# Optimization experiments

Hardware: AMD Instinct MI355X
Metric: run time of the kernel (lower is better)

The kernel has to match this reference:

```python
import jax, jax.numpy as jnp
import numpy as np

TIME_WEIGHT = 0.1
CURRENT_TIME = 0.0

def setup_inputs() -> dict:
    key = jax.random.key(0)
    k1, k2, k3, k4, k5 = jax.random.split(key, 5)
    B, M, D, C = 131072, 100, 1024, 16
    return {
        "query": jax.random.normal(k1, (B, D), dtype=jnp.float32),
        "context": jax.random.normal(k2, (B, C), dtype=jnp.float32),
        "mem_keys": jax.random.normal(k3, (M, D), dtype=jnp.float32),
        "mem_values": jax.random.normal(k4, (M, D), dtype=jnp.float32),
        "mem_contexts": jax.random.normal(k5, (M, C), dtype=jnp.float32),
        "mem_timestamps": jnp.zeros((M, 1), dtype=jnp.float32),
    }

def reference(query, context, mem_keys, mem_values, mem_contexts, mem_timestamps):
    # content scores: [B, M]
    scores = jnp.einsum('bd,md->bm', query, mem_keys)
    # contextual binding
    scores = scores + 0.5 * jnp.einsum('bc,mc->bm', context, mem_contexts)
    # exponential time-decay bias, broadcast over batch: [M]
    time_decay = jnp.exp(-TIME_WEIGHT * (CURRENT_TIME - mem_timestamps.squeeze(-1)))
    scores = scores + time_decay[None, :]
    attn = jax.nn.softmax(scores, axis=-1)
    return jnp.einsum('bm,md->bd', attn, mem_values)
```

## Files before the change

kernel.cpp:

```cpp
#include <hip/hip_runtime.h>


typedef __attribute__((ext_vector_type(8))) _Float16 f16x8;
typedef __attribute__((ext_vector_type(4))) float f32x4;

constexpr int DQ = 1024, CD = 16, MM = 100, KD = 1056, NT = 7;
constexpr size_t KE = (size_t)112 * KD;

constexpr int KOFF = 8192, KBUF = 7168;
constexpr int VOFF = 32768, VBUF = 8192;
constexpr int LDSZ = 57344;

#define WAITV(n) asm volatile("s_waitcnt vmcnt(" #n ")" ::: "memory")

__device__ __forceinline__ void gl16(const void* g, void* l) {
    __builtin_amdgcn_global_load_lds(
        (const __attribute__((address_space(1))) unsigned int*)g,
        (__attribute__((address_space(3))) unsigned int*)l, 16, 0, 0);
}

__global__ void build_k(const float* __restrict__ mk, const float* __restrict__ mc,
                        _Float16* __restrict__ KH)
{
    int d = blockIdx.x * 64 + threadIdx.x;
    int m = blockIdx.y;
    if (d >= KD) return;
    float x = 0.f;
    if (m < MM) {
        if (d < DQ)            x = mk[(size_t)m * DQ + d];
        else if (d < DQ + CD)  x = 0.5f * mc[(size_t)m * CD + (d - DQ)];
    }
    KH[(size_t)m * KD + d] = (_Float16)x;
}

__global__ void build_vt(const float* __restrict__ mv, _Float16* __restrict__ VT)
{
    int idx = blockIdx.x * 256 + threadIdx.x;
    int d = idx >> 7, m = idx & 127;
    VT[idx] = (m < MM) ? (_Float16)mv[(size_t)m * DQ + d] : (_Float16)0.f;
}

__global__ __launch_bounds__(512, 4)
void epmem_pipe(const float* __restrict__ q, const float* __restrict__ cx,
                const float* __restrict__ ts,
                const _Float16* __restrict__ KH, const _Float16* __restrict__ VT,
                float* __restrict__ out)
{
    __shared__ __align__(16) char lds[LDSZ];

    const int t = threadIdx.x, w = t >> 6, lane = t & 63;
    const int lr = lane & 15, lk = lane >> 4;
    const int row0 = blockIdx.x * 128;

    float dec[NT];
    #pragma unroll
    for (int nt = 0; nt < NT; ++nt) {
        int m = nt * 16 + lr;
        dec[nt] = (m < MM) ? __expf(0.1f * ts[m]) : 0.f;
    }

    auto stageCtx = [&]() {
        gl16(cx + (size_t)(row0 + (t >> 2)) * CD + (t & 3) * 4, lds + (w * 64) * 16);
    };
    auto stageK = [&](int buf, int ks) {
        if (w < 7) {
            char* dst = lds + KOFF + buf * KBUF;
            int s = w * 64 + lane;
            int m = s >> 2;
            int logical = (s & 3) ^ ((m >> 1) & 3);
            gl16(KH + (size_t)m * KD + ks * 32 + logical * 8, dst + (w * 64) * 16);
        }
    };
    auto stageV = [&](int buf, int c) {
        char* dst = lds + VOFF + buf * VBUF;
        int d = t >> 4;
        int logical = (t & 15) ^ (d & 15);
        gl16(VT + (size_t)(c * 32 + d) * 128 + logical * 8, dst + (w * 64) * 16);
    };

    f32x4 acc[NT];
    #pragma unroll
    for (int nt = 0; nt < NT; ++nt) acc[nt] = (f32x4){0.f, 0.f, 0.f, 0.f};

    const float* qp = q + (size_t)(row0 + w * 16 + lr) * DQ + 8 * lk;

    auto qkStep = [&](f32x4 x, f32x4 y, int ks) {
        f16x8 ah, al;
        #pragma unroll
        for (int e = 0; e < 4; ++e) {
            _Float16 h = (_Float16)x[e]; ah[e] = h;     al[e] = (_Float16)(x[e] - (float)h);
            h = (_Float16)y[e];          ah[4 + e] = h; al[4 + e] = (_Float16)(y[e] - (float)h);
        }
        const char* kb = lds + KOFF + (ks % 3) * KBUF;
        #pragma unroll
        for (int nt = 0; nt < NT; ++nt) {
            int m = nt * 16 + lr;
            f16x8 bh = *(const f16x8*)(kb + ((m << 2) + (lk ^ ((lr >> 1) & 3))) * 16);
            acc[nt] = __builtin_amdgcn_mfma_f32_16x16x32_f16(ah, bh, acc[nt], 0, 0, 0);
            acc[nt] = __builtin_amdgcn_mfma_f32_16x16x32_f16(al, bh, acc[nt], 0, 0, 0);
        }
    };

    stageCtx();
    stageK(0, 0); stageK(1, 1);
    f32x4 qA0 = __builtin_nontemporal_load((const f32x4*)(qp + 0));
    f32x4 qA1 = __builtin_nontemporal_load((const f32x4*)(qp + 4));
    f32x4 qB0 = __builtin_nontemporal_load((const f32x4*)(qp + 32));
    f32x4 qB1 = __builtin_nontemporal_load((const f32x4*)(qp + 36));
    WAITV(0);
    __builtin_amdgcn_s_barrier();

    for (int ks = 0; ks < 32; ks += 2) {
        stageK((ks + 2) % 3, ks + 2);
        f32x4 nx0, nx1;
        if (ks <= 28) {
            nx0 = __builtin_nontemporal_load((const f32x4*)(qp + (ks + 2) * 32));
            nx1 = __builtin_nontemporal_load((const f32x4*)(qp + (ks + 2) * 32 + 4));
        }
        qkStep(qA0, qA1, ks);
        if (ks <= 28) { qA0 = nx0; qA1 = nx1; }
        if (ks <= 28) { if (w < 7) { WAITV(3); } else { WAITV(2); } }
        else          { if (w < 7) { WAITV(1); } else { WAITV(0); } }
        __builtin_amdgcn_s_barrier();

        if (ks <= 28) stageK((ks + 3) % 3, ks + 3);
        f32x4 ny0, ny1;
        if (ks <= 28) {
            ny0 = __builtin_nontemporal_load((const f32x4*)(qp + (ks + 3) * 32));
            ny1 = __builtin_nontemporal_load((const f32x4*)(qp + (ks + 3) * 32 + 4));
        }
        qkStep(qB0, qB1, ks + 1);
        if (ks <= 28) { qB0 = ny0; qB1 = ny1; }
        if (ks <= 28) { if (w < 7) { WAITV(3); } else { WAITV(2); } }
        else          { WAITV(0); }
        __builtin_amdgcn_s_barrier();
    }

    {
        f16x8 ah, al;
        if (lk < 2) {
            const char* base = lds + (w * 16 + lr) * 64;
            f32x4 x = *(const f32x4*)(base + (2 * lk) * 16);
            f32x4 y = *(const f32x4*)(base + (2 * lk + 1) * 16);
            #pragma unroll
            for (int e = 0; e < 4; ++e) {
                _Float16 h = (_Float16)x[e]; ah[e] = h;     al[e] = (_Float16)(x[e] - (float)h);
                h = (_Float16)y[e];          ah[4 + e] = h; al[4 + e] = (_Float16)(y[e] - (float)h);
            }
        } else {
            #pragma unroll
            for (int e = 0; e < 8; ++e) { ah[e] = (_Float16)0.f; al[e] = (_Float16)0.f; }
        }
        const char* kb = lds + KOFF + 2 * KBUF;
        #pragma unroll
        for (int nt = 0; nt < NT; ++nt) {
            int m = nt * 16 + lr;
            f16x8 bh = *(const f16x8*)(kb + ((m << 2) + (lk ^ ((lr >> 1) & 3))) * 16);
            acc[nt] = __builtin_amdgcn_mfma_f32_16x16x32_f16(ah, bh, acc[nt], 0, 0, 0);
            acc[nt] = __builtin_amdgcn_mfma_f32_16x16x32_f16(al, bh, acc[nt], 0, 0, 0);
        }
    }
    __syncthreads();

    stageV(0, 0); stageV(1, 1);

    char* Pb = lds + w * 4096;
    {
        float rm[4] = {-3e38f, -3e38f, -3e38f, -3e38f};
        #pragma unroll
        for (int nt = 0; nt < NT; ++nt) {
            int m = nt * 16 + lr;
            #pragma unroll
            for (int r = 0; r < 4; ++r) {
                float s = (m < MM) ? (acc[nt][r] + dec[nt]) : -3e38f;
                acc[nt][r] = s;
                rm[r] = fmaxf(rm[r], s);
            }
        }
        #pragma unroll
        for (int r = 0; r < 4; ++r)
            #pragma unroll
            for (int off = 1; off < 16; off <<= 1)
                rm[r] = fmaxf(rm[r], __shfl_xor(rm[r], off));
        float rs[4] = {0.f, 0.f, 0.f, 0.f};
        #pragma unroll
        for (int nt = 0; nt < NT; ++nt)
            #pragma unroll
            for (int r = 0; r < 4; ++r) {
                float e = __expf(acc[nt][r] - rm[r]);
                acc[nt][r] = e;
                rs[r] += e;
            }
        #pragma unroll
        for (int r = 0; r < 4; ++r)
            #pragma unroll
            for (int off = 1; off < 16; off <<= 1)
                rs[r] += __shfl_xor(rs[r], off);
        #pragma unroll
        for (int r = 0; r < 4; ++r) {
            float inv = 1.f / rs[r];
            int row = 4 * lk + r;
            #pragma unroll
            for (int nt = 0; nt < NT; ++nt)
                *(_Float16*)(Pb + row * 256 + (((nt * 2 + (lr >> 3)) ^ row) & 15) * 16
                             + (lr & 7) * 2) = (_Float16)(acc[nt][r] * inv);
        }
    }
    if (lane < 32) {
        int row = lane >> 1, sl = 14 + (lane & 1);
        uint4 z = {0u, 0u, 0u, 0u};
        *(uint4*)(Pb + row * 256 + ((sl ^ row) & 15) * 16) = z;
    }
    WAITV(1);
    __builtin_amdgcn_s_barrier();

    f16x8 pa[4];
    #pragma unroll
    for (int k4 = 0; k4 < 4; ++k4)
        pa[k4] = *(const f16x8*)(Pb + lr * 256 + (((k4 * 4 + lk) ^ lr) & 15) * 16);

    int vc = 0;
    for (int c = 0; c < 32; ++c) {
        int vs = vc + 2; if (vs >= 3) vs -= 3;
        if (c + 2 < 32) stageV(vs, c + 2);
        f32x4 o0 = {0.f, 0.f, 0.f, 0.f}, o1 = {0.f, 0.f, 0.f, 0.f};
        #pragma unroll
        for (int k4 = 0; k4 < 4; ++k4) {
            const char* vb = lds + VOFF + vc * VBUF + (((k4 * 4 + lk) ^ lr) & 15) * 16;
            f16x8 b0 = *(const f16x8*)(vb + lr * 256);
            f16x8 b1 = *(const f16x8*)(vb + (16 + lr) * 256);
            o0 = __builtin_amdgcn_mfma_f32_16x16x32_f16(pa[k4], b0, o0, 0, 0, 0);
            o1 = __builtin_amdgcn_mfma_f32_16x16x32_f16(pa[k4], b1, o1, 0, 0, 0);
        }
        #pragma unroll
        for (int r = 0; r < 4; ++r) {
            size_t rw = (size_t)(row0 + w * 16 + 4 * lk + r) * DQ + c * 32;
            __builtin_nontemporal_store(o0[r], &out[rw + lr]);
            __builtin_nontemporal_store(o1[r], &out[rw + 16 + lr]);
        }
        if (c == 0)       { WAITV(9); }
        else if (c <= 29) { WAITV(17); }
        else if (c == 30) { WAITV(16); }
        if (c < 31) __builtin_amdgcn_s_barrier();
        if (++vc == 3) vc = 0;
    }
}

extern "C" void kernel_launch(void* const* d_in, const int* in_sizes, int n_in,
                              void* d_out, int out_size, void* d_ws, size_t ws_size,
                              hipStream_t stream) {
    const float* q  = (const float*)d_in[0];
    const float* cx = (const float*)d_in[1];
    const float* mk = (const float*)d_in[2];
    const float* mv = (const float*)d_in[3];
    const float* mc = (const float*)d_in[4];
    const float* ts = (const float*)d_in[5];
    float* out = (float*)d_out;

    _Float16* wsp = (_Float16*)d_ws;
    _Float16* KH = wsp;
    _Float16* VT = wsp + KE;

    const int B = in_sizes[0] / DQ;

    build_k<<<dim3(17, 112), dim3(64), 0, stream>>>(mk, mc, KH);
    build_vt<<<dim3(512), dim3(256), 0, stream>>>(mv, VT);
    epmem_pipe<<<dim3(B / 128), dim3(512), 0, stream>>>(q, cx, ts, KH, VT, out);
}
```

Measured before the change: 317.7 us.

## Stage query tiles through LDS with async loads and halve block size

Query rows are now staged into double-buffered, swizzled LDS tiles with global_load_lds instead of being loaded straight into registers per lane. Blocks shrink to 64 rows and 4 waves, with K staging spread across fewer waves. V chunks widen to 64 columns so each step issues four MFMAs. The goal is to overlap the large query stream with compute through async LDS loads, at the cost of higher LDS use per block (64KB), which limits occupancy, and retuned waitcnt bookkeeping that is easy to get wrong.

```diff
diff --git a/kernel.cpp b/kernel.cpp
--- a/kernel.cpp
+++ b/kernel.cpp
@@ -7,9 +7,9 @@
 constexpr int DQ = 1024, CD = 16, MM = 100, KD = 1056, NT = 7;
 constexpr size_t KE = (size_t)112 * KD;
 
-constexpr int KOFF = 8192, KBUF = 7168;
-constexpr int VOFF = 32768, VBUF = 8192;
-constexpr int LDSZ = 57344;
+constexpr int QBUF = 16384, KOFF = 32768, KBUF = 7168;
+constexpr int VOFF = 16384, VBUF = 16384;
+constexpr int LDSZ = 65536;
 
 #define WAITV(n) asm volatile("s_waitcnt vmcnt(" #n ")" ::: "memory")
 
@@ -40,7 +40,7 @@
     VT[idx] = (m < MM) ? (_Float16)mv[(size_t)m * DQ + d] : (_Float16)0.f;
 }
 
-__global__ __launch_bounds__(512, 4)
+__global__ __launch_bounds__(256, 2)
 void epmem_pipe(const float* __restrict__ q, const float* __restrict__ cx,
                 const float* __restrict__ ts,
                 const _Float16* __restrict__ KH, const _Float16* __restrict__ VT,
@@ -50,7 +50,7 @@
 
     const int t = threadIdx.x, w = t >> 6, lane = t & 63;
     const int lr = lane & 15, lk = lane >> 4;
-    const int row0 = blockIdx.x * 128;
+    const int row0 = blockIdx.x * 64;
 
     float dec[NT];
     #pragma unroll
@@ -59,39 +59,54 @@
         dec[nt] = (m < MM) ? __expf(0.1f * ts[m]) : 0.f;
     }
 
-    auto stageCtx = [&]() {
-        gl16(cx + (size_t)(row0 + (t >> 2)) * CD + (t & 3) * 4, lds + (w * 64) * 16);
+    auto stageQ = [&](int buf, int ms) {
+        char* dst = lds + buf * QBUF;
+        #pragma unroll
+        for (int i = 0; i < 4; ++i) {
+            int s = i * 256 + t;
+            int row = s >> 4;
+            int logical = (s & 15) ^ (row & 15);
+            gl16(q + (size_t)(row0 + row) * DQ + ms * 64 + logical * 4,
+                 dst + (i * 256 + w * 64) * 16);
+        }
+    };
+    auto stageQctx = [&](int buf) {
+        char* dst = lds + buf * QBUF;
+        gl16(cx + (size_t)(row0 + (t >> 2)) * CD + (t & 3) * 4, dst + (w * 64) * 16);
     };
     auto stageK = [&](int buf, int ks) {
-        if (w < 7) {
-            char* dst = lds + KOFF + buf * KBUF;
-            int s = w * 64 + lane;
+        char* dst = lds + KOFF + buf * KBUF;
+        for (int i = w; i < 7; i += 4) {
+            int s = i * 64 + lane;
             int m = s >> 2;
             int logical = (s & 3) ^ ((m >> 1) & 3);
-            gl16(KH + (size_t)m * KD + ks * 32 + logical * 8, dst + (w * 64) * 16);
+            gl16(KH + (size_t)m * KD + ks * 32 + logical * 8, dst + (i * 64) * 16);
         }
     };
     auto stageV = [&](int buf, int c) {
         char* dst = lds + VOFF + buf * VBUF;
-        int d = t >> 4;
-        int logical = (t & 15) ^ (d & 15);
-        gl16(VT + (size_t)(c * 32 + d) * 128 + logical * 8, dst + (w * 64) * 16);
+        #pragma unroll
+        for (int i = 0; i < 4; ++i) {
+            int s = i * 256 + t;
+            int d = s >> 4;
+            int logical = (s & 15) ^ (d & 15);
+            gl16(VT + (size_t)(c * 64 + d) * 128 + logical * 8,
+                 dst + (i * 256 + w * 64) * 16);
+        }
     };
 
     f32x4 acc[NT];
     #pragma unroll
     for (int nt = 0; nt < NT; ++nt) acc[nt] = (f32x4){0.f, 0.f, 0.f, 0.f};
 
-    const float* qp = q + (size_t)(row0 + w * 16 + lr) * DQ + 8 * lk;
-
-    auto qkStep = [&](f32x4 x, f32x4 y, int ks) {
+    auto qkStep = [&](const char* qx, const char* qy, const char* kb) {
+        f32x4 x = *(const f32x4*)qx, y = *(const f32x4*)qy;
         f16x8 ah, al;
         #pragma unroll
         for (int e = 0; e < 4; ++e) {
             _Float16 h = (_Float16)x[e]; ah[e] = h;     al[e] = (_Float16)(x[e] - (float)h);
             h = (_Float16)y[e];          ah[4 + e] = h; al[4 + e] = (_Float16)(y[e] - (float)h);
         }
-        const char* kb = lds + KOFF + (ks % 3) * KBUF;
         #pragma unroll
         for (int nt = 0; nt < NT; ++nt) {
             int m = nt * 16 + lr;
@@ -101,41 +116,33 @@
         }
     };
 
-    stageCtx();
+    stageQ(0, 0);
     stageK(0, 0); stageK(1, 1);
-    f32x4 qA0 = __builtin_nontemporal_load((const f32x4*)(qp + 0));
-    f32x4 qA1 = __builtin_nontemporal_load((const f32x4*)(qp + 4));
-    f32x4 qB0 = __builtin_nontemporal_load((const f32x4*)(qp + 32));
-    f32x4 qB1 = __builtin_nontemporal_load((const f32x4*)(qp + 36));
-    WAITV(0);
+    if (w < 3) { WAITV(2); } else { WAITV(1); }
     __builtin_amdgcn_s_barrier();
 
-    for (int ks = 0; ks < 32; ks += 2) {
-        stageK((ks + 2) % 3, ks + 2);
-        f32x4 nx0, nx1;
-        if (ks <= 28) {
-            nx0 = __builtin_nontemporal_load((const f32x4*)(qp + (ks + 2) * 32));
-            nx1 = __builtin_nontemporal_load((const f32x4*)(qp + (ks + 2) * 32 + 4));
-        }
-        qkStep(qA0, qA1, ks);
-        if (ks <= 28) { qA0 = nx0; qA1 = nx1; }
-        if (ks <= 28) { if (w < 7) { WAITV(3); } else { WAITV(2); } }
-        else          { if (w < 7) { WAITV(1); } else { WAITV(0); } }
+    for (int ss = 0; ss < 32; ++ss) {
+        const int ms = ss >> 1, h = ss & 1;
+        if (h == 0) {
+            if (ms + 1 <= 15)   stageQ((ms + 1) & 1, ms + 1);
+            else                stageQctx(0);
+        }
+        if (ss <= 30) stageK((ss + 2) % 3, ss + 2);
+
+        const char* base = lds + (ms & 1) * QBUF + (w * 16 + lr) * 256;
+        const int u0 = h * 8 + 2 * lk;
+        qkStep(base + ((u0 ^ lr) << 4), base + (((u0 + 1) ^ lr) << 4),
+               lds + KOFF + (ss % 3) * KBUF);
+
+        if (h == 0) {
+            if (ss == 30) { if (w < 3) { WAITV(3); } else { WAITV(2); } }
+            else          { if (w < 3) { WAITV(6); } else { WAITV(5); } }
+        } else {
+            if (ss == 31) { WAITV(0); }
+            else          { if (w < 3) { WAITV(2); } else { WAITV(1); } }
+        }
         __builtin_amdgcn_s_barrier();
-
-        if (ks <= 28) stageK((ks + 3) % 3, ks + 3);
-        f32x4 ny0, ny1;
-        if (ks <= 28) {
-            ny0 = __builtin_nontemporal_load((const f32x4*)(qp + (ks + 3) * 32));
-            ny1 = __builtin_nontemporal_load((const f32x4*)(qp + (ks + 3) * 32 + 4));
-        }
-        qkStep(qB0, qB1, ks + 1);
-        if (ks <= 28) { qB0 = ny0; qB1 = ny1; }
-        if (ks <= 28) { if (w < 7) { WAITV(3); } else { WAITV(2); } }
-        else          { WAITV(0); }
-        __builtin_amdgcn_s_barrier();
-    }
-
+    }
     {
         f16x8 ah, al;
         if (lk < 2) {
@@ -211,7 +218,7 @@
         uint4 z = {0u, 0u, 0u, 0u};
         *(uint4*)(Pb + row * 256 + ((sl ^ row) & 15) * 16) = z;
     }
-    WAITV(1);
+    WAITV(4);
     __builtin_amdgcn_s_barrier();
 
     f16x8 pa[4];
@@ -219,30 +226,35 @@
     for (int k4 = 0; k4 < 4; ++k4)
         pa[k4] = *(const f16x8*)(Pb + lr * 256 + (((k4 * 4 + lk) ^ lr) & 15) * 16);
 
-    int vc = 0;
-    for (int c = 0; c < 32; ++c) {
-        int vs = vc + 2; if (vs >= 3) vs -= 3;
-        if (c + 2 < 32) stageV(vs, c + 2);
-        f32x4 o0 = {0.f, 0.f, 0.f, 0.f}, o1 = {0.f, 0.f, 0.f, 0.f};
+    for (int c = 0; c < 16; ++c) {
+        if (c + 2 < 16) stageV((c + 2) % 3, c + 2);
+        const char* vb = lds + VOFF + (c % 3) * VBUF;
+        f32x4 o0 = {0.f,0.f,0.f,0.f}, o1 = {0.f,0.f,0.f,0.f};
+        f32x4 o2 = {0.f,0.f,0.f,0.f}, o3 = {0.f,0.f,0.f,0.f};
         #pragma unroll
         for (int k4 = 0; k4 < 4; ++k4) {
-            const char* vb = lds + VOFF + vc * VBUF + (((k4 * 4 + lk) ^ lr) & 15) * 16;
-            f16x8 b0 = *(const f16x8*)(vb + lr * 256);
-            f16x8 b1 = *(const f16x8*)(vb + (16 + lr) * 256);
+            const char* vb2 = vb + (((k4 * 4 + lk) ^ lr) & 15) * 16;
+            f16x8 b0 = *(const f16x8*)(vb2 + lr * 256);
+            f16x8 b1 = *(const f16x8*)(vb2 + (16 + lr) * 256);
+            f16x8 b2 = *(const f16x8*)(vb2 + (32 + lr) * 256);
+            f16x8 b3 = *(const f16x8*)(vb2 + (48 + lr) * 256);
             o0 = __builtin_amdgcn_mfma_f32_16x16x32_f16(pa[k4], b0, o0, 0, 0, 0);
             o1 = __builtin_amdgcn_mfma_f32_16x16x32_f16(pa[k4], b1, o1, 0, 0, 0);
+            o2 = __builtin_amdgcn_mfma_f32_16x16x32_f16(pa[k4], b2, o2, 0, 0, 0);
+            o3 = __builtin_amdgcn_mfma_f32_16x16x32_f16(pa[k4], b3, o3, 0, 0, 0);
         }
         #pragma unroll
         for (int r = 0; r < 4; ++r) {
-            size_t rw = (size_t)(row0 + w * 16 + 4 * lk + r) * DQ + c * 32;
+            size_t rw = (size_t)(row0 + w * 16 + 4 * lk + r) * DQ + c * 64;
             __builtin_nontemporal_store(o0[r], &out[rw + lr]);
             __builtin_nontemporal_store(o1[r], &out[rw + 16 + lr]);
-        }
-        if (c == 0)       { WAITV(9); }
-        else if (c <= 29) { WAITV(17); }
-        else if (c == 30) { WAITV(16); }
-        if (c < 31) __builtin_amdgcn_s_barrier();
-        if (++vc == 3) vc = 0;
+            __builtin_nontemporal_store(o2[r], &out[rw + 32 + lr]);
+            __builtin_nontemporal_store(o3[r], &out[rw + 48 + lr]);
+        }
+        if (c == 0)       { WAITV(20); }
+        else if (c <= 13) { WAITV(36); }
+        else if (c == 14) { WAITV(32); }
+        if (c < 15) __builtin_amdgcn_s_barrier();
     }
 }
 
@@ -265,5 +277,5 @@
 
     build_k<<<dim3(17, 112), dim3(64), 0, stream>>>(mk, mc, KH);
     build_vt<<<dim3(512), dim3(256), 0, stream>>>(mv, VT);
-    epmem_pipe<<<dim3(B / 128), dim3(512), 0, stream>>>(q, cx, ts, KH, VT, out);
-}
+    epmem_pipe<<<dim3(B / 64), dim3(256), 0, stream>>>(q, cx, ts, KH, VT, out);
+}
```

New measurement: 270.3 us. 1.18x faster.
